# Kernel tuning notes

Hardware: AMD Instinct MI355X
Metric: run time of the kernel (lower is better)

## Reference

```python
import jax, jax.numpy as jnp
import numpy as np

GR = 16

def _conv(x, w, b, pad):
    y = jax.lax.conv_general_dilated(x, w, (1, 1), [(pad, pad), (pad, pad)],
                                     dimension_numbers=('NCHW', 'OIHW', 'NCHW'))
    return y + b[None, :, None, None]

def _build_stencil(h, w):
    num = h * w
    a = np.zeros((num, 4, num), np.float32)
    i = np.arange(num)
    m0 = ((i + 1) % w != 0) & (i + 1 < num)
    a[i[m0], 0, i[m0]] = 1.0; a[i[m0], 0, i[m0] + 1] = -1.0
    m1 = i + w < num
    a[i[m1], 1, i[m1]] = 1.0; a[i[m1], 1, i[m1] + w] = -1.0
    m2 = ((i + 2) % w != 0) & (i + 2 < num)
    a[i[m2], 2, i[m2]] = 1.0; a[i[m2], 2, i[m2] + 2] = -1.0
    m3 = i + 2 * w < num
    a[i[m3], 3, i[m3]] = 1.0; a[i[m3], 3, i[m3] + 2 * w] = -1.0
    a[-1, 0, -1] = 1.0; a[-1, 1, -1] = 1.0; a[-1, 2, -1] = 1.0; a[-1, 3, -1] = 1.0
    return jnp.asarray(a)  # (num, 4, num)

def setup_inputs() -> dict:
    key = jax.random.key(0)
    ks = jax.random.split(key, 20)
    n, c, h, w = 4, 64, 24, 24
    s = 0.02
    inp = {
        'x': jax.random.normal(ks[0], (n, c, h, w), jnp.float32),
        'a': _build_stencil(h, w),
        'grad_w1': jax.random.normal(ks[1], (c, c, 3, 3)) * s,
        'grad_b1': jnp.zeros((c,)),
        'grad_w2': jax.random.normal(ks[2], (4 * GR, c, 3, 3)) * s,
        'grad_b2': jnp.zeros((4 * GR,)),
        'att_w1': jax.random.normal(ks[3], (c, c, 3, 3)) * s,
        'att_b1': jnp.zeros((c,)),
        'att_w2': jax.random.normal(ks[4], (4 * GR, c, 3, 3)) * s,
        'att_b2': jnp.zeros((4 * GR,)),
        'se_w1': jax.random.normal(ks[5], (c // 2, c, 1, 1)) * s,
        'se_b1': jnp.zeros((c // 2,)),
        'se_w2': jax.random.normal(ks[6], (GR, c // 2, 1, 1)) * s,
        'se_b2': jnp.zeros((GR,)),
        'gn_w': jnp.ones((GR,)),
        'gn_b': jnp.zeros((GR,)),
        'post_w': jax.random.normal(ks[7], (8 * GR, GR, 3, 3)) * s,
        'post_b': jnp.zeros((8 * GR,)),
    }
    return inp

def reference(x, a, grad_w1, grad_b1, grad_w2, grad_b2,
              att_w1, att_b1, att_w2, att_b2,
              se_w1, se_b1, se_w2, se_b2,
              gn_w, gn_b, post_w, post_b):
    n, c, h, w = x.shape
    num = h * w
    # attention branch: conv -> leaky_relu -> conv -> sigmoid
    att = jax.nn.sigmoid(_conv(jax.nn.leaky_relu(_conv(x, att_w1, att_b1, 1), 0.01), att_w2, att_b2, 1))
    # gradient branch: conv -> leaky_relu -> conv
    grad = _conv(jax.nn.leaky_relu(_conv(x, grad_w1, grad_b1, 1), 0.01), grad_w2, grad_b2, 1)
    # squeeze-excite: GAP -> 1x1 conv -> leaky -> 1x1 conv -> sigmoid
    pooled = x.mean(axis=(2, 3), keepdims=True)  # (n,c,1,1)
    se = jax.nn.sigmoid(_conv(jax.nn.leaky_relu(_conv(pooled, se_w1, se_b1, 0), 0.01), se_w2, se_b2, 0))
    # reshape per-pixel 4-tap weights: (n*GR, num, 4, 1)
    att_r = att.reshape(n * GR, 4, num, 1).transpose(0, 2, 1, 3)
    grad_r = grad.reshape(n * GR, 4, num, 1).transpose(0, 2, 1, 3)
    # densified weighted stencil operator
    A = a[None] * att_r                      # (b, num, 4, num)
    B = (grad_r * att_r)[..., 0]             # (b, num, 4)
    A = A.reshape(n * GR, num * 4, num)      # (b, 4num, num)
    B = B.reshape(n * GR, num * 4)           # (b, 4num)
    ATA = jnp.einsum('bkn,bkm->bnm', A, A)   # (b, num, num)
    ATB = jnp.einsum('bkn,bk->bn', A, B)[..., None]
    ATA = ATA + jnp.eye(num, dtype=x.dtype)[None] * 1e-12
    sol = jnp.linalg.solve(ATA, ATB)         # (b, num, 1)
    y = sol.reshape(n, GR, h, w)
    # GroupNorm(1, GR): normalize over all channels + spatial, eps=1e-5
    mu = y.mean(axis=(1, 2, 3), keepdims=True)
    var = y.var(axis=(1, 2, 3), keepdims=True)
    y = (y - mu) / jnp.sqrt(var + 1e-5)
    y = y * gn_w[None, :, None, None] + gn_b[None, :, None, None]
    y = se * y
    return _conv(y, post_w, post_b, 1)
```

## Files before the change

kernel.cpp:

```cpp
#include <hip/hip_runtime.h>
#include <math.h>

#define NUM 576
#define BSTR 50
#define CTH 512
#define CHOL_LDS_BYTES ((NUM * BSTR + CTH) * sizeof(float))

__device__ __forceinline__ float leakyf(float v) { return v > 0.f ? v : 0.01f * v; }
__device__ __forceinline__ float sigmoidf(float v) { return 1.f / (1.f + __expf(-v)); }
__device__ __forceinline__ float rdlane(float v, int l) {
  return __uint_as_float(__builtin_amdgcn_readlane(__float_as_uint(v), l));
}

__global__ __launch_bounds__(576) void conv1se_kernel(
    const float* __restrict__ x,
    const float* __restrict__ wa, const float* __restrict__ ba,
    const float* __restrict__ wg, const float* __restrict__ bg,
    const float* __restrict__ sw1, const float* __restrict__ sb1,
    const float* __restrict__ sw2, const float* __restrict__ sb2,
    float* __restrict__ outa, float* __restrict__ outg,
    float* __restrict__ sev, double* __restrict__ acc)
{
  __shared__ float sx[16 * 576];
  __shared__ float pooled[64];
  __shared__ float hid[32];
  const int co = blockIdx.x, n = blockIdx.y;
  const int tid = threadIdx.x;

  if (co == 64) {
    if (tid < 2) acc[n * 2 + tid] = 0.0;
    if (tid < 64) {
      const float4* xp4 = (const float4*)(x + (size_t)(n * 64 + tid) * 576);
      float s = 0.f;
      for (int p = 0; p < 144; ++p) {
        float4 v = xp4[p];
        s += v.x + v.y + v.z + v.w;
      }
      pooled[tid] = s * (1.f / 576.f);
    }
    __syncthreads();
    if (tid < 32) {
      float h = sb1[tid];
      for (int c = 0; c < 64; ++c) h += pooled[c] * sw1[tid * 64 + c];
      hid[tid] = leakyf(h);
    }
    __syncthreads();
    if (tid < 16) {
      float v = sb2[tid];
      for (int j = 0; j < 32; ++j) v += hid[j] * sw2[tid * 32 + j];
      sev[n * 16 + tid] = sigmoidf(v);
    }
    return;
  }

  const int py = tid / 24, px = tid - py * 24;
  float acc_a = ba[co];
  float acc_g = bg[co];
  for (int c0 = 0; c0 < 64; c0 += 16) {
    __syncthreads();
    {
      const float4* xs4 = (const float4*)(x + (size_t)(n * 64 + c0) * 576);
      float4* sx4 = (float4*)sx;
#pragma unroll
      for (int q = 0; q < 4; ++q) sx4[tid + q * 576] = xs4[tid + q * 576];
    }
    __syncthreads();
#pragma unroll 4
    for (int k = 0; k < 16; ++k) {
      const float* wpa = wa + (co * 64 + c0 + k) * 9;
      const float* wpg = wg + (co * 64 + c0 + k) * 9;
#pragma unroll
      for (int dy = 0; dy < 3; ++dy) {
        const int yy = py + dy - 1;
        const bool oky = (unsigned)yy < 24u;
        const int iy = yy < 0 ? 0 : (yy > 23 ? 23 : yy);
#pragma unroll
        for (int dx = 0; dx < 3; ++dx) {
          const int xx = px + dx - 1;
          const bool ok = oky && ((unsigned)xx < 24u);
          const int ix = xx < 0 ? 0 : (xx > 23 ? 23 : xx);
          const float v = ok ? sx[k * 576 + iy * 24 + ix] : 0.f;
          acc_a += v * wpa[dy * 3 + dx];
          acc_g += v * wpg[dy * 3 + dx];
        }
      }
    }
  }
  const int o = (n * 64 + co) * 576 + tid;
  outa[o] = leakyf(acc_a);
  outg[o] = leakyf(acc_g);
}

__global__ __launch_bounds__(576) void conv2_kernel(
    const float* __restrict__ t1a, const float* __restrict__ t1g,
    const float* __restrict__ wa, const float* __restrict__ ba,
    const float* __restrict__ wg, const float* __restrict__ bg,
    float* __restrict__ att, float* __restrict__ grd)
{
  __shared__ float sx[16 * 576];
  const int co = blockIdx.x, n = blockIdx.y, br = blockIdx.z;
  const float* src = br ? t1g : t1a;
  const float* wp0 = br ? wg : wa;
  const float bias = br ? bg[co] : ba[co];
  float* dst = br ? grd : att;
  const int tid = threadIdx.x;
  const int py = tid / 24, px = tid - py * 24;
  float acc = bias;
  for (int c0 = 0; c0 < 64; c0 += 16) {
    __syncthreads();
    {
      const float4* s4 = (const float4*)(src + (size_t)(n * 64 + c0) * 576);
      float4* sx4 = (float4*)sx;
#pragma unroll
      for (int q = 0; q < 4; ++q) sx4[tid + q * 576] = s4[tid + q * 576];
    }
    __syncthreads();
#pragma unroll 4
    for (int k = 0; k < 16; ++k) {
      const float* wp = wp0 + (co * 64 + c0 + k) * 9;
#pragma unroll
      for (int dy = 0; dy < 3; ++dy) {
        const int yy = py + dy - 1;
        const bool oky = (unsigned)yy < 24u;
        const int iy = yy < 0 ? 0 : (yy > 23 ? 23 : yy);
#pragma unroll
        for (int dx = 0; dx < 3; ++dx) {
          const int xx = px + dx - 1;
          const bool ok = oky && ((unsigned)xx < 24u);
          const int ix = xx < 0 ? 0 : (xx > 23 ? 23 : xx);
          const float v = ok ? sx[k * 576 + iy * 24 + ix] : 0.f;
          acc += v * wp[dy * 3 + dx];
        }
      }
    }
  }
  if (br == 0) acc = sigmoidf(acc);
  dst[(n * 64 + co) * 576 + tid] = acc;
}

__global__ __launch_bounds__(CTH, 1) void chol_kernel(
    const float* __restrict__ att, const float* __restrict__ grd,
    float* __restrict__ sol, double* __restrict__ acc)
{
  extern __shared__ float S[];
  __shared__ float RHS_s[NUM];
  __shared__ float RD_s[NUM];
  __shared__ float XS_s[NUM];
  __shared__ __align__(16) float CP[8][64];
  __shared__ float DUMW[64];
  __shared__ double RW[16];
  const int b = blockIdx.x, tid = threadIdx.x;
  const int n = b >> 4, g = b & 15;
  const float* ac = att + (size_t)(n * 64 + g * 4) * 576;
  const float* gc = grd + (size_t)(n * 64 + g * 4) * 576;

  int r1A, r2A;
  {
    const int T = (tid < 300) ? tid : 0;
    int U = (int)((sqrtf(8.f * (float)T + 1.f) - 1.f) * 0.5f);
    while (U * (U + 1) / 2 > T) --U;
    while ((U + 1) * (U + 2) / 2 <= T) ++U;
    const int W = T - U * (U + 1) / 2;
    r1A = (tid < 300) ? (8 + 2 * U) : 63;
    r2A = 8 + 2 * W;
  }

  for (int i = tid; i < NUM * BSTR; i += CTH) S[i] = 0.f;
  __syncthreads();

  for (int i = tid; i < NUM; i += CTH) {
    float diag = 1e-12f, rv = 0.f;
    float od1 = 0.f, od2 = 0.f, od24 = 0.f, od48 = 0.f;
    if (((i + 1) % 24 != 0) && (i + 1 < NUM)) {
      float a0 = ac[0 * 576 + i]; float s = a0 * a0;
      diag += s; rv += s * gc[0 * 576 + i];
    }
    if (i - 1 >= 0 && (i % 24 != 0)) {
      float a0 = ac[0 * 576 + (i - 1)]; float s = a0 * a0;
      diag += s; rv -= s * gc[0 * 576 + (i - 1)]; od1 = -s;
    }
    if (i + 24 < NUM) {
      float a1 = ac[1 * 576 + i]; float s = a1 * a1;
      diag += s; rv += s * gc[1 * 576 + i];
    }
    if (i - 24 >= 0) {
      float a1 = ac[1 * 576 + (i - 24)]; float s = a1 * a1;
      diag += s; rv -= s * gc[1 * 576 + (i - 24)]; od24 = -s;
    }
    if (((i + 2) % 24 != 0) && (i + 2 < NUM)) {
      float a2 = ac[2 * 576 + i]; float s = a2 * a2;
      diag += s; rv += s * gc[2 * 576 + i];
    }
    if (i - 2 >= 0 && (i % 24 != 0)) {
      float a2 = ac[2 * 576 + (i - 2)]; float s = a2 * a2;
      diag += s; rv -= s * gc[2 * 576 + (i - 2)]; od2 = -s;
    }
    if (i + 48 < NUM) {
      float a3 = ac[3 * 576 + i]; float s = a3 * a3;
      diag += s; rv += s * gc[3 * 576 + i];
    }
    if (i - 48 >= 0) {
      float a3 = ac[3 * 576 + (i - 48)]; float s = a3 * a3;
      diag += s; rv -= s * gc[3 * 576 + (i - 48)]; od48 = -s;
    }
    if (i == NUM - 1) {
#pragma unroll
      for (int t = 0; t < 4; ++t) {
        float a = ac[t * 576 + (NUM - 1)]; float s = a * a;
        diag += s; rv += s * gc[t * 576 + (NUM - 1)];
      }
    }
    S[i * BSTR + 0] = diag;
    S[i * BSTR + 1] = od1;
    S[i * BSTR + 2] = od2;
    S[i * BSTR + 24] = od24;
    S[i * BSTR + 48] = od48;
    RHS_s[i] = rv;
    if (i == 0) RD_s[0] = rsqrtf(diag);
  }

  for (int j = 0; j < NUM; j += 8) {
    __syncthreads();
    if (tid < 64) {
      const int t = tid;
      const int row = j + t;
      const bool rok = row < NUM;
      float v[8];
#pragma unroll
      for (int c = 0; c < 8; ++c) {
        const bool okc = rok && (t >= c) && (t - c <= 48);
        const int addr = okc ? (row * BSTR + (t - c)) : (NUM * BSTR + t);
        float vv = S[addr];
        v[c] = okc ? vv : 0.f;
      }
      float zb[8];
#pragma unroll
      for (int k = 0; k < 8; ++k) zb[k] = RHS_s[j + k];
      float z = RHS_s[rok ? row : j];
      z = rok ? z : 0.f;
      const float rd0 = RD_s[j];
      float rdv[8], y[8], lp[8][8];
#pragma unroll
      for (int k = 0; k < 8; ++k) {
        if (k == 0) {
          rdv[0] = rd0;
        } else {
          const float dk = rdlane(v[k], k);
          rdv[k] = rsqrtf(dk);
        }
        v[k] *= rdv[k];
#pragma unroll
        for (int m = k + 1; m < 8; ++m) {
          lp[m][k] = rdlane(v[k], m);
          v[m] -= v[k] * lp[m][k];
        }
      }
      y[0] = zb[0] * rdv[0];
#pragma unroll
      for (int k = 1; k < 8; ++k) {
        float a = zb[k];
#pragma unroll
        for (int m = 0; m < 8; ++m)
          if (m < k) a -= lp[k][m] * y[m];
        y[k] = a * rdv[k];
      }
      float zn = z;
#pragma unroll
      for (int c = 0; c < 8; ++c) zn -= v[c] * y[c];
#pragma unroll
      for (int c = 0; c < 8; ++c) {
        const bool okc = rok && (t > c) && (t - c <= 48);
        float* bp = okc ? &S[row * BSTR + (t - c)] : &S[NUM * BSTR + t];
        *bp = v[c];
        CP[c][t] = okc ? v[c] : 0.f;
      }
      if (t < 8) {
        float yv = y[0], rv = rdv[0];
#pragma unroll
        for (int k = 1; k < 8; ++k) {
          yv = (t == k) ? y[k] : yv;
          rv = (t == k) ? rdv[k] : rv;
        }
        RHS_s[row] = yv;
        RD_s[row] = rv;
      } else {
        float* rp = rok ? &RHS_s[row] : &DUMW[t & 63];
        *rp = zn;
      }
    }
    __syncthreads();
    const int R = (NUM - 1) - j;
    {
      const bool a0 = (r1A <= R);
      const bool a1 = (r1A + 1 <= R);
      float2 cr[8], cc[8];
#pragma unroll
      for (int c = 0; c < 8; ++c) {
        cr[c] = *(const float2*)&CP[c][r1A & 62];
        cc[c] = *(const float2*)&CP[c][r2A];
      }
      float s00 = 0.f, s01 = 0.f, s10 = 0.f, s11 = 0.f;
#pragma unroll
      for (int c = 0; c < 8; ++c) {
        s00 += cr[c].x * cc[c].x; s01 += cr[c].x * cc[c].y;
        s10 += cr[c].y * cc[c].x; s11 += cr[c].y * cc[c].y;
      }
      const int p00 = j * BSTR + 51 * r1A - r2A;
      float* q00 = a0 ? &S[p00] : &S[NUM * BSTR + tid];
      float* q01 = a0 ? &S[p00 - 1] : &S[NUM * BSTR + tid];
      float* q10 = a1 ? &S[p00 + 51] : &S[NUM * BSTR + tid];
      float* q11 = a1 ? &S[p00 + 50] : &S[NUM * BSTR + tid];
      const float t00 = *q00 - s00, t01 = *q01 - s01;
      const float t10 = *q10 - s10, t11 = *q11 - s11;
      *q00 = t00; *q01 = t01; *q10 = t10; *q11 = t11;
      if (tid == 0 && a0)
        RD_s[j + 8] = rsqrtf(t00);
    }
  }
  __syncthreads();

  if (tid < 64) {
    const int t = tid;
    for (int i = NUM - 1; i >= 7; i -= 8) {
      asm volatile("s_waitcnt lgkmcnt(0)" ::: "memory");
      float zz[8], rr[8];
#pragma unroll
      for (int k = 0; k < 8; ++k) { zz[k] = RHS_s[i - k]; rr[k] = RD_s[i - k]; }
      float L[8][8];
#pragma unroll
      for (int a = 0; a < 8; ++a)
#pragma unroll
        for (int bb = 0; bb < 8; ++bb)
          if (bb > a) L[a][bb] = S[(i - a) * BSTR + (bb - a)];
      float x[8];
      x[0] = zz[0] * rr[0];
#pragma unroll
      for (int k = 1; k < 8; ++k) {
        float a = zz[k];
#pragma unroll
        for (int m = 0; m < 8; ++m)
          if (m < k) a -= L[m][k] * x[m];
        x[k] = a * rr[k];
      }
      const int rb = i - 8 - t;
      const bool bok = rb >= 0;
      float acc2 = 0.f;
#pragma unroll
      for (int k = 0; k < 8; ++k) {
        const int d = 8 + t - k;
        const bool ok = bok && (d <= 48);
        float Lv = S[ok ? ((i - k) * BSTR + d) : (NUM * BSTR + t)];
        Lv = ok ? Lv : 0.f;
        acc2 += Lv * x[k];
      }
      const float zbv = RHS_s[bok ? rb : 0];
      float* rp = bok ? &RHS_s[rb] : &DUMW[t];
      *rp = zbv - acc2;
      float xv = x[0];
#pragma unroll
      for (int k = 1; k < 8; ++k) xv = (t == k) ? x[k] : xv;
      if (t < 8) XS_s[i - t] = xv;
    }
  }
  __syncthreads();

  double ls = 0.0, ls2 = 0.0;
  for (int i = tid; i < NUM; i += CTH) {
    const float xv = XS_s[i];
    sol[(size_t)b * NUM + i] = xv;
    ls += (double)xv;
    ls2 += (double)xv * (double)xv;
  }
#pragma unroll
  for (int off = 32; off > 0; off >>= 1) {
    ls += __shfl_down(ls, off);
    ls2 += __shfl_down(ls2, off);
  }
  if ((tid & 63) == 0) {
    RW[(tid >> 6) * 2] = ls;
    RW[(tid >> 6) * 2 + 1] = ls2;
  }
  __syncthreads();
  if (tid == 0) {
    double s = 0.0, s2 = 0.0;
#pragma unroll
    for (int wv = 0; wv < 8; ++wv) { s += RW[wv * 2]; s2 += RW[wv * 2 + 1]; }
    atomicAdd(&acc[n * 2], s);
    atomicAdd(&acc[n * 2 + 1], s2);
  }
}

__global__ __launch_bounds__(576) void postgn_kernel(
    const float* __restrict__ sol, const double* __restrict__ acc,
    const float* __restrict__ sev,
    const float* __restrict__ gnw, const float* __restrict__ gnb,
    const float* __restrict__ w, const float* __restrict__ bias,
    float* __restrict__ out)
{
  __shared__ float sy[16 * 576];
  const int co = blockIdx.x, n = blockIdx.y, tid = threadIdx.x;
  const double mu_d = acc[n * 2] * (1.0 / 9216.0);
  const double var_d = acc[n * 2 + 1] * (1.0 / 9216.0) - mu_d * mu_d;
  const float rstd = (float)(1.0 / sqrt(var_d + 1e-5));
  const float muf = (float)mu_d;
  {
    const float4* sp4 = (const float4*)(sol + (size_t)n * 9216);
    float4* sy4 = (float4*)sy;
#pragma unroll
    for (int q = 0; q < 4; ++q) {
      const int p = tid + q * 576;
      const int k = p / 144;
      const float sv = sev[n * 16 + k];
      const float A = rstd * gnw[k] * sv;
      const float B = (gnb[k] - muf * rstd * gnw[k]) * sv;
      float4 v = sp4[p];
      v.x = v.x * A + B; v.y = v.y * A + B;
      v.z = v.z * A + B; v.w = v.w * A + B;
      sy4[p] = v;
    }
  }
  __syncthreads();
  const int py = tid / 24, px = tid - py * 24;
  float a = bias[co];
#pragma unroll 4
  for (int k = 0; k < 16; ++k) {
    const float* wp = w + (co * 16 + k) * 9;
#pragma unroll
    for (int dy = 0; dy < 3; ++dy) {
      const int yy = py + dy - 1;
      const bool oky = (unsigned)yy < 24u;
      const int iy = yy < 0 ? 0 : (yy > 23 ? 23 : yy);
#pragma unroll
      for (int dx = 0; dx < 3; ++dx) {
        const int xx = px + dx - 1;
        const bool ok = oky && ((unsigned)xx < 24u);
        const int ix = xx < 0 ? 0 : (xx > 23 ? 23 : xx);
        const float v = ok ? sy[k * 576 + iy * 24 + ix] : 0.f;
        a += v * wp[dy * 3 + dx];
      }
    }
  }
  out[(size_t)(n * 128 + co) * 576 + tid] = a;
}

extern "C" void kernel_launch(void* const* d_in, const int* in_sizes, int n_in,
                              void* d_out, int out_size, void* d_ws, size_t ws_size,
                              hipStream_t stream) {
  const float* x       = (const float*)d_in[0];
  const float* grad_w1 = (const float*)d_in[2];
  const float* grad_b1 = (const float*)d_in[3];
  const float* grad_w2 = (const float*)d_in[4];
  const float* grad_b2 = (const float*)d_in[5];
  const float* att_w1  = (const float*)d_in[6];
  const float* att_b1  = (const float*)d_in[7];
  const float* att_w2  = (const float*)d_in[8];
  const float* att_b2  = (const float*)d_in[9];
  const float* se_w1   = (const float*)d_in[10];
  const float* se_b1   = (const float*)d_in[11];
  const float* se_w2   = (const float*)d_in[12];
  const float* se_b2   = (const float*)d_in[13];
  const float* gn_w    = (const float*)d_in[14];
  const float* gn_b    = (const float*)d_in[15];
  const float* post_w  = (const float*)d_in[16];
  const float* post_b  = (const float*)d_in[17];
  float* out = (float*)d_out;

  float* ws  = (float*)d_ws;
  float* t1a = ws;
  float* t1g = t1a + 147456;
  float* att = t1g + 147456;
  float* grd = att + 147456;
  float* sev = grd + 147456;
  float* sol = sev + 64;
  double* acc = (double*)(sol + 36864);

  (void)hipFuncSetAttribute((const void*)chol_kernel,
                            hipFuncAttributeMaxDynamicSharedMemorySize,
                            (int)CHOL_LDS_BYTES);

  conv1se_kernel<<<dim3(65, 4), 576, 0, stream>>>(
      x, att_w1, att_b1, grad_w1, grad_b1,
      se_w1, se_b1, se_w2, se_b2, t1a, t1g, sev, acc);
  conv2_kernel<<<dim3(64, 4, 2), 576, 0, stream>>>(t1a, t1g, att_w2, att_b2,
                                                   grad_w2, grad_b2, att, grd);
  chol_kernel<<<64, CTH, CHOL_LDS_BYTES, stream>>>(att, grd, sol, acc);
  postgn_kernel<<<dim3(128, 4), 576, 0, stream>>>(sol, acc, sev, gn_w, gn_b,
                                                  post_w, post_b, out);
}
```

Before: 198.8 us.

## Pad conv tiles with zero halos and pipeline Cholesky trailing updates

The three conv kernels now stage inputs into a zero-padded 26x26 shared-memory tile, which removes the per-tap bounds checks and clamps. The Cholesky factorisation double-buffers the column panel so that a near set of 90 threads updates the immediate block while other threads apply the far trailing update from the previous panel, overlapping it with the next panel factorisation. The back substitution is software-pipelined by prefetching the next block's L, diagonal and tail values into registers. The cost is more register pressure and LDS usage, plus scalar (non-vectorised) LDS stores when filling the padded tiles.

```diff
diff --git a/kernel.cpp b/kernel.cpp
--- a/kernel.cpp
+++ b/kernel.cpp
@@ -21,7 +21,7 @@
     float* __restrict__ outa, float* __restrict__ outg,
     float* __restrict__ sev, double* __restrict__ acc)
 {
-  __shared__ float sx[16 * 576];
+  __shared__ float sx[16 * 676];
   __shared__ float pooled[64];
   __shared__ float hid[32];
   const int co = blockIdx.x, n = blockIdx.y;
@@ -54,36 +54,37 @@
   }
 
   const int py = tid / 24, px = tid - py * 24;
+  const int hb0 = py * 26 + px;
+  for (int i = tid; i < 16 * 676; i += 576) sx[i] = 0.f;
   float acc_a = ba[co];
   float acc_g = bg[co];
   for (int c0 = 0; c0 < 64; c0 += 16) {
     __syncthreads();
-    {
-      const float4* xs4 = (const float4*)(x + (size_t)(n * 64 + c0) * 576);
-      float4* sx4 = (float4*)sx;
-#pragma unroll
-      for (int q = 0; q < 4; ++q) sx4[tid + q * 576] = xs4[tid + q * 576];
+#pragma unroll
+    for (int q = 0; q < 4; ++q) {
+      const int p = tid + q * 576;
+      const int k = p / 144;
+      const int r = p - k * 144;
+      const int pix = r * 4;
+      const int ppy = pix / 24, ppx = pix - ppy * 24;
+      const float4 v = *(const float4*)&x[(size_t)(n * 64 + c0) * 576 + p * 4];
+      float* d = &sx[k * 676 + (ppy + 1) * 26 + ppx + 1];
+      d[0] = v.x; d[1] = v.y; d[2] = v.z; d[3] = v.w;
     }
     __syncthreads();
 #pragma unroll 4
     for (int k = 0; k < 16; ++k) {
       const float* wpa = wa + (co * 64 + c0 + k) * 9;
       const float* wpg = wg + (co * 64 + c0 + k) * 9;
-#pragma unroll
-      for (int dy = 0; dy < 3; ++dy) {
-        const int yy = py + dy - 1;
-        const bool oky = (unsigned)yy < 24u;
-        const int iy = yy < 0 ? 0 : (yy > 23 ? 23 : yy);
+      const float* sp = &sx[k * 676 + hb0];
+#pragma unroll
+      for (int dy = 0; dy < 3; ++dy)
 #pragma unroll
         for (int dx = 0; dx < 3; ++dx) {
-          const int xx = px + dx - 1;
-          const bool ok = oky && ((unsigned)xx < 24u);
-          const int ix = xx < 0 ? 0 : (xx > 23 ? 23 : xx);
-          const float v = ok ? sx[k * 576 + iy * 24 + ix] : 0.f;
+          const float v = sp[dy * 26 + dx];
           acc_a += v * wpa[dy * 3 + dx];
           acc_g += v * wpg[dy * 3 + dx];
         }
-      }
     }
   }
   const int o = (n * 64 + co) * 576 + tid;
@@ -97,7 +98,7 @@
     const float* __restrict__ wg, const float* __restrict__ bg,
     float* __restrict__ att, float* __restrict__ grd)
 {
-  __shared__ float sx[16 * 576];
+  __shared__ float sx[16 * 676];
   const int co = blockIdx.x, n = blockIdx.y, br = blockIdx.z;
   const float* src = br ? t1g : t1a;
   const float* wp0 = br ? wg : wa;
@@ -105,38 +106,84 @@
   float* dst = br ? grd : att;
   const int tid = threadIdx.x;
   const int py = tid / 24, px = tid - py * 24;
+  const int hb0 = py * 26 + px;
+  for (int i = tid; i < 16 * 676; i += 576) sx[i] = 0.f;
   float acc = bias;
   for (int c0 = 0; c0 < 64; c0 += 16) {
     __syncthreads();
-    {
-      const float4* s4 = (const float4*)(src + (size_t)(n * 64 + c0) * 576);
-      float4* sx4 = (float4*)sx;
-#pragma unroll
-      for (int q = 0; q < 4; ++q) sx4[tid + q * 576] = s4[tid + q * 576];
+#pragma unroll
+    for (int q = 0; q < 4; ++q) {
+      const int p = tid + q * 576;
+      const int k = p / 144;
+      const int r = p - k * 144;
+      const int pix = r * 4;
+      const int ppy = pix / 24, ppx = pix - ppy * 24;
+      const float4 v = *(const float4*)&src[(size_t)(n * 64 + c0) * 576 + p * 4];
+      float* d = &sx[k * 676 + (ppy + 1) * 26 + ppx + 1];
+      d[0] = v.x; d[1] = v.y; d[2] = v.z; d[3] = v.w;
     }
     __syncthreads();
 #pragma unroll 4
     for (int k = 0; k < 16; ++k) {
       const float* wp = wp0 + (co * 64 + c0 + k) * 9;
-#pragma unroll
-      for (int dy = 0; dy < 3; ++dy) {
-        const int yy = py + dy - 1;
-        const bool oky = (unsigned)yy < 24u;
-        const int iy = yy < 0 ? 0 : (yy > 23 ? 23 : yy);
-#pragma unroll
-        for (int dx = 0; dx < 3; ++dx) {
-          const int xx = px + dx - 1;
-          const bool ok = oky && ((unsigned)xx < 24u);
-          const int ix = xx < 0 ? 0 : (xx > 23 ? 23 : xx);
-          const float v = ok ? sx[k * 576 + iy * 24 + ix] : 0.f;
-          acc += v * wp[dy * 3 + dx];
-        }
-      }
+      const float* sp = &sx[k * 676 + hb0];
+#pragma unroll
+      for (int dy = 0; dy < 3; ++dy)
+#pragma unroll
+        for (int dx = 0; dx < 3; ++dx)
+          acc += sp[dy * 26 + dx] * wp[dy * 3 + dx];
     }
   }
   if (br == 0) acc = sigmoidf(acc);
   dst[(n * 64 + co) * 576 + tid] = acc;
 }
+
+#define BS_LOAD(ip, L, rr, tl)                                                \
+  {                                                                           \
+    _Pragma("unroll")                                                         \
+    for (int a = 0; a < 8; ++a)                                               \
+      _Pragma("unroll")                                                       \
+      for (int bb = a + 1; bb < 8; ++bb)                                      \
+        L[a][bb] = S[((ip) - a) * BSTR + (bb - a)];                           \
+    _Pragma("unroll")                                                         \
+    for (int k = 0; k < 8; ++k) rr[k] = RD_s[(ip) - k];                       \
+    _Pragma("unroll")                                                         \
+    for (int k = 0; k < 8; ++k) {                                             \
+      const int d = 8 + t - k;                                                \
+      tl[k] = (d <= 48) ? S[((ip) - k) * BSTR + d] : 0.f;                     \
+    }                                                                         \
+  }
+
+#define BS_STEP(i, L, rr, tl, ipre, Lp, rrp, tlp)                             \
+  {                                                                           \
+    asm volatile("s_waitcnt lgkmcnt(0)" ::: "memory");                        \
+    float zz[8];                                                              \
+    _Pragma("unroll")                                                         \
+    for (int k = 0; k < 8; ++k) zz[k] = RHS_s[(i) - k];                       \
+    const int rb = (i) - 8 - t;                                               \
+    const bool bok = rb >= 0;                                                 \
+    const float zbv = RHS_s[bok ? rb : 0];                                    \
+    if ((ipre) >= 7) BS_LOAD(ipre, Lp, rrp, tlp);                             \
+    float xx[8];                                                              \
+    xx[0] = zz[0] * rr[0];                                                    \
+    _Pragma("unroll")                                                         \
+    for (int k = 1; k < 8; ++k) {                                             \
+      float a2 = zz[k];                                                       \
+      _Pragma("unroll")                                                       \
+      for (int m = 0; m < 8; ++m)                                             \
+        if (m < k) a2 -= L[m][k] * xx[m];                                     \
+      xx[k] = a2 * rr[k];                                                     \
+    }                                                                         \
+    float at = 0.f;                                                           \
+    _Pragma("unroll")                                                         \
+    for (int k = 0; k < 8; ++k) at += tl[k] * xx[k];                          \
+    float* rp = bok ? &RHS_s[rb] : &DUMW[t];                                  \
+    *rp = zbv - at;                                                           \
+    float xv = xx[0];                                                         \
+    _Pragma("unroll")                                                         \
+    for (int k = 1; k < 8; ++k) xv = (t == k) ? xx[k] : xv;                   \
+    if (t < 8) XS_s[(i) - t] = xv;                                            \
+  }
 
 __global__ __launch_bounds__(CTH, 1) void chol_kernel(
     const float* __restrict__ att, const float* __restrict__ grd,
@@ -146,7 +193,7 @@
   __shared__ float RHS_s[NUM];
   __shared__ float RD_s[NUM];
   __shared__ float XS_s[NUM];
-  __shared__ __align__(16) float CP[8][64];
+  __shared__ __align__(16) float CP[2][8][64];
   __shared__ float DUMW[64];
   __shared__ double RW[16];
   const int b = blockIdx.x, tid = threadIdx.x;
@@ -154,15 +201,29 @@
   const float* ac = att + (size_t)(n * 64 + g * 4) * 576;
   const float* gc = grd + (size_t)(n * 64 + g * 4) * 576;
 
-  int r1A, r2A;
+  int r1C, r2C;
+  const bool okC = tid < 90;
   {
-    const int T = (tid < 300) ? tid : 0;
-    int U = (int)((sqrtf(8.f * (float)T + 1.f) - 1.f) * 0.5f);
-    while (U * (U + 1) / 2 > T) --U;
-    while ((U + 1) * (U + 2) / 2 <= T) ++U;
-    const int W = T - U * (U + 1) / 2;
-    r1A = (tid < 300) ? (8 + 2 * U) : 63;
-    r2A = 8 + 2 * W;
+    const int idx = okC ? tid : 0;
+    int U, W;
+    if (idx < 6) {
+      U = (idx == 0) ? 0 : (idx < 3) ? 1 : 2;
+      W = idx - U * (U + 1) / 2;
+    } else {
+      U = 3 + (idx - 6) / 4;
+      W = (idx - 6) & 3;
+    }
+    r1C = 8 + 2 * U; r2C = 8 + 2 * W;
+  }
+  int r1N, r2N;
+  const bool okN = (tid >= 64) && (tid < 64 + 210);
+  {
+    const int idx = okN ? (tid - 64) : 0;
+    int k = (int)((sqrtf(8.f * (float)idx + 1.f) - 1.f) * 0.5f);
+    while (k * (k + 1) / 2 > idx) --k;
+    while ((k + 1) * (k + 2) / 2 <= idx) ++k;
+    const int w = idx - k * (k + 1) / 2;
+    r1N = 8 + 2 * (k + 4); r2N = 8 + 2 * (w + 4);
   }
 
   for (int i = tid; i < NUM * BSTR; i += CTH) S[i] = 0.f;
@@ -218,9 +279,10 @@
     RHS_s[i] = rv;
     if (i == 0) RD_s[0] = rsqrtf(diag);
   }
+  __syncthreads();
 
   for (int j = 0; j < NUM; j += 8) {
-    __syncthreads();
+    const int p = (j >> 3) & 1;
     if (tid < 64) {
       const int t = tid;
       const int row = j + t;
@@ -272,7 +334,7 @@
         const bool okc = rok && (t > c) && (t - c <= 48);
         float* bp = okc ? &S[row * BSTR + (t - c)] : &S[NUM * BSTR + t];
         *bp = v[c];
-        CP[c][t] = okc ? v[c] : 0.f;
+        CP[p][c][t] = okc ? v[c] : 0.f;
       }
       if (t < 8) {
         float yv = y[0], rv = rdv[0];
@@ -287,17 +349,44 @@
         float* rp = rok ? &RHS_s[row] : &DUMW[t & 63];
         *rp = zn;
       }
-    }
-    __syncthreads();
-    const int R = (NUM - 1) - j;
+    } else {
+      const int jp = j - 8;
+      if (jp >= 0) {
+        const int Rp = (NUM - 1) - jp;
+        const bool a0 = okN && (r1N <= Rp);
+        const bool a1 = okN && (r1N + 1 <= Rp);
+        float2 cr[8], cc[8];
+#pragma unroll
+        for (int c = 0; c < 8; ++c) {
+          cr[c] = *(const float2*)&CP[p ^ 1][c][r1N];
+          cc[c] = *(const float2*)&CP[p ^ 1][c][r2N];
+        }
+        float s00 = 0.f, s01 = 0.f, s10 = 0.f, s11 = 0.f;
+#pragma unroll
+        for (int c = 0; c < 8; ++c) {
+          s00 += cr[c].x * cc[c].x; s01 += cr[c].x * cc[c].y;
+          s10 += cr[c].y * cc[c].x; s11 += cr[c].y * cc[c].y;
+        }
+        const int p00 = jp * BSTR + 51 * r1N - r2N;
+        float* q00 = a0 ? &S[p00] : &S[NUM * BSTR + tid];
+        float* q01 = a0 ? &S[p00 - 1] : &S[NUM * BSTR + tid];
+        float* q10 = a1 ? &S[p00 + 51] : &S[NUM * BSTR + tid];
+        float* q11 = a1 ? &S[p00 + 50] : &S[NUM * BSTR + tid];
+        const float t00 = *q00 - s00, t01 = *q01 - s01;
+        const float t10 = *q10 - s10, t11 = *q11 - s11;
+        *q00 = t00; *q01 = t01; *q10 = t10; *q11 = t11;
+      }
+    }
+    __syncthreads();
     {
-      const bool a0 = (r1A <= R);
-      const bool a1 = (r1A + 1 <= R);
+      const int R = (NUM - 1) - j;
+      const bool a0 = okC && (r1C <= R);
+      const bool a1 = okC && (r1C + 1 <= R);
       float2 cr[8], cc[8];
 #pragma unroll
       for (int c = 0; c < 8; ++c) {
-        cr[c] = *(const float2*)&CP[c][r1A & 62];
-        cc[c] = *(const float2*)&CP[c][r2A];
+        cr[c] = *(const float2*)&CP[p][c][r1C];
+        cc[c] = *(const float2*)&CP[p][c][r2C];
       }
       float s00 = 0.f, s01 = 0.f, s10 = 0.f, s11 = 0.f;
 #pragma unroll
@@ -305,7 +394,7 @@
         s00 += cr[c].x * cc[c].x; s01 += cr[c].x * cc[c].y;
         s10 += cr[c].y * cc[c].x; s11 += cr[c].y * cc[c].y;
       }
-      const int p00 = j * BSTR + 51 * r1A - r2A;
+      const int p00 = j * BSTR + 51 * r1C - r2C;
       float* q00 = a0 ? &S[p00] : &S[NUM * BSTR + tid];
       float* q01 = a0 ? &S[p00 - 1] : &S[NUM * BSTR + tid];
       float* q10 = a1 ? &S[p00 + 51] : &S[NUM * BSTR + tid];
@@ -316,50 +405,16 @@
       if (tid == 0 && a0)
         RD_s[j + 8] = rsqrtf(t00);
     }
-  }
-  __syncthreads();
+    __syncthreads();
+  }
 
   if (tid < 64) {
     const int t = tid;
-    for (int i = NUM - 1; i >= 7; i -= 8) {
-      asm volatile("s_waitcnt lgkmcnt(0)" ::: "memory");
-      float zz[8], rr[8];
-#pragma unroll
-      for (int k = 0; k < 8; ++k) { zz[k] = RHS_s[i - k]; rr[k] = RD_s[i - k]; }
-      float L[8][8];
-#pragma unroll
-      for (int a = 0; a < 8; ++a)
-#pragma unroll
-        for (int bb = 0; bb < 8; ++bb)
-          if (bb > a) L[a][bb] = S[(i - a) * BSTR + (bb - a)];
-      float x[8];
-      x[0] = zz[0] * rr[0];
-#pragma unroll
-      for (int k = 1; k < 8; ++k) {
-        float a = zz[k];
-#pragma unroll
-        for (int m = 0; m < 8; ++m)
-          if (m < k) a -= L[m][k] * x[m];
-        x[k] = a * rr[k];
-      }
-      const int rb = i - 8 - t;
-      const bool bok = rb >= 0;
-      float acc2 = 0.f;
-#pragma unroll
-      for (int k = 0; k < 8; ++k) {
-        const int d = 8 + t - k;
-        const bool ok = bok && (d <= 48);
-        float Lv = S[ok ? ((i - k) * BSTR + d) : (NUM * BSTR + t)];
-        Lv = ok ? Lv : 0.f;
-        acc2 += Lv * x[k];
-      }
-      const float zbv = RHS_s[bok ? rb : 0];
-      float* rp = bok ? &RHS_s[rb] : &DUMW[t];
-      *rp = zbv - acc2;
-      float xv = x[0];
-#pragma unroll
-      for (int k = 1; k < 8; ++k) xv = (t == k) ? x[k] : xv;
-      if (t < 8) XS_s[i - t] = xv;
+    float LA[8][8], LB[8][8], rrA[8], rrB[8], tlA[8], tlB[8];
+    BS_LOAD(NUM - 1, LA, rrA, tlA);
+    for (int i = NUM - 1; i >= 15; i -= 16) {
+      BS_STEP(i, LA, rrA, tlA, i - 8, LB, rrB, tlB);
+      BS_STEP(i - 8, LB, rrB, tlB, i - 16, LA, rrA, tlA);
     }
   }
   __syncthreads();
@@ -397,48 +452,43 @@
     const float* __restrict__ w, const float* __restrict__ bias,
     float* __restrict__ out)
 {
-  __shared__ float sy[16 * 576];
+  __shared__ float sy[16 * 676];
   const int co = blockIdx.x, n = blockIdx.y, tid = threadIdx.x;
   const double mu_d = acc[n * 2] * (1.0 / 9216.0);
   const double var_d = acc[n * 2 + 1] * (1.0 / 9216.0) - mu_d * mu_d;
   const float rstd = (float)(1.0 / sqrt(var_d + 1e-5));
   const float muf = (float)mu_d;
-  {
-    const float4* sp4 = (const float4*)(sol + (size_t)n * 9216);
-    float4* sy4 = (float4*)sy;
-#pragma unroll
-    for (int q = 0; q < 4; ++q) {
-      const int p = tid + q * 576;
-      const int k = p / 144;
-      const float sv = sev[n * 16 + k];
-      const float A = rstd * gnw[k] * sv;
-      const float B = (gnb[k] - muf * rstd * gnw[k]) * sv;
-      float4 v = sp4[p];
-      v.x = v.x * A + B; v.y = v.y * A + B;
-      v.z = v.z * A + B; v.w = v.w * A + B;
-      sy4[p] = v;
-    }
+  for (int i = tid; i < 16 * 676; i += 576) sy[i] = 0.f;
+  __syncthreads();
+#pragma unroll
+  for (int q = 0; q < 4; ++q) {
+    const int p = tid + q * 576;
+    const int k = p / 144;
+    const int r = p - k * 144;
+    const int pix = r * 4;
+    const int ppy = pix / 24, ppx = pix - ppy * 24;
+    const float sv = sev[n * 16 + k];
+    const float gw = gnw[k] * rstd;
+    const float A = gw * sv;
+    const float B = (gnb[k] - muf * gw) * sv;
+    const float4 v = *(const float4*)&sol[(size_t)n * 9216 + p * 4];
+    float* d = &sy[k * 676 + (ppy + 1) * 26 + ppx + 1];
+    d[0] = v.x * A + B; d[1] = v.y * A + B;
+    d[2] = v.z * A + B; d[3] = v.w * A + B;
   }
   __syncthreads();
   const int py = tid / 24, px = tid - py * 24;
+  const int hb0 = py * 26 + px;
   float a = bias[co];
 #pragma unroll 4
   for (int k = 0; k < 16; ++k) {
     const float* wp = w + (co * 16 + k) * 9;
-#pragma unroll
-    for (int dy = 0; dy < 3; ++dy) {
-      const int yy = py + dy - 1;
-      const bool oky = (unsigned)yy < 24u;
-      const int iy = yy < 0 ? 0 : (yy > 23 ? 23 : yy);
-#pragma unroll
-      for (int dx = 0; dx < 3; ++dx) {
-        const int xx = px + dx - 1;
-        const bool ok = oky && ((unsigned)xx < 24u);
-        const int ix = xx < 0 ? 0 : (xx > 23 ? 23 : xx);
-        const float v = ok ? sy[k * 576 + iy * 24 + ix] : 0.f;
-        a += v * wp[dy * 3 + dx];
-      }
-    }
+    const float* sp = &sy[k * 676 + hb0];
+#pragma unroll
+    for (int dy = 0; dy < 3; ++dy)
+#pragma unroll
+      for (int dx = 0; dx < 3; ++dx)
+        a += sp[dy * 26 + dx] * wp[dy * 3 + dx];
   }
   out[(size_t)(n * 128 + co) * 576 + tid] = a;
 }
```

Measured after the change: 206.3 us. 3.8% more time.
